# Kernel tuning notes

Hardware: AMD Instinct MI355X
Metric: run time of the kernel (lower is better)

## Reference

```python
import jax, jax.numpy as jnp
import numpy as np

N_NODES = 50000
N_EDGES = 500000
D_NODE = 128
D_EDGE = 64
D_HID = 256
D_OUT = 64


def setup_inputs() -> dict:
    key = jax.random.key(0)
    k1, k2, k3, k4, k5 = jax.random.split(key, 5)
    node_feats = jax.random.normal(k1, (N_NODES, D_NODE), dtype=jnp.float32)
    edge_index = jax.random.randint(k2, (2, N_EDGES), 0, N_NODES, dtype=jnp.int64)
    edge_attr = jax.random.normal(k3, (N_EDGES, D_EDGE), dtype=jnp.float32)
    d_in = 2 * D_NODE + D_EDGE  # 320
    W1 = jax.random.normal(k4, (d_in, D_HID), dtype=jnp.float32) * (1.0 / np.sqrt(d_in))
    b1 = jnp.zeros((D_HID,), dtype=jnp.float32)
    W2 = jax.random.normal(k5, (D_HID, D_OUT), dtype=jnp.float32) * (1.0 / np.sqrt(D_HID))
    b2 = jnp.zeros((D_OUT,), dtype=jnp.float32)
    return {"node_feats": node_feats, "edge_index": edge_index, "edge_attr": edge_attr,
            "W1": W1, "b1": b1, "W2": W2, "b2": b2}


def reference(node_feats, edge_index, edge_attr, W1, b1, W2, b2):
    row, col = edge_index[0], edge_index[1]
    # irregular gather of endpoint features, concat with edge attrs: [E, 2*d_node + d_edge]
    x = jnp.concatenate([node_feats[row], node_feats[col], edge_attr], axis=1)
    h = jax.nn.relu(x @ W1 + b1)  # [E, D_HID]
    return h @ W2 + b2            # [E, D_OUT]
```

## Files before the change

### kernel.cpp

```cpp
#include <hip/hip_runtime.h>
#include <hip/hip_bf16.h>
#include <stdint.h>

#define E_EDGES 500000
#define NNODES  50000
#define DN 128
#define DE 64
#define DH 256
#define DO 64
#define BE 32

typedef __attribute__((ext_vector_type(8))) short short8;
typedef __attribute__((ext_vector_type(4))) short short4v;
typedef __attribute__((ext_vector_type(4))) float f32x4;

__device__ __forceinline__ short f2bf(float f) {
    union { float f; uint32_t u; } v; v.f = f;
    uint32_t r = (v.u + 0x7FFFu + ((v.u >> 16) & 1u)) >> 16;
    return (short)(uint16_t)r;
}
__device__ __forceinline__ float bf2f(short s) {
    union { uint32_t u; float f; } v; v.u = ((uint32_t)(uint16_t)s) << 16;
    return v.f;
}

__global__ void convert_weights(const float* __restrict__ W1, const float* __restrict__ W2,
                                short* __restrict__ WcatT, short* __restrict__ W1cT,
                                short* __restrict__ W2T) {
    int idx = blockIdx.x * 256 + threadIdx.x;
    if (idx < 512 * 128) {
        int c = idx >> 7, k = idx & 127;
        WcatT[idx] = f2bf(W1[(c < 256 ? k : k + 128) * DH + (c & 255)]);
    } else if (idx < 512 * 128 + 256 * 64) {
        int i = idx - 512 * 128;
        int c = i >> 6, k = i & 63;
        W1cT[i] = f2bf(W1[(256 + k) * DH + c]);
    } else if (idx < 512 * 128 + 256 * 64 + 64 * 256) {
        int i = idx - 512 * 128 - 256 * 64;
        int n = i >> 8, k = i & 255;
        W2T[i] = f2bf(W2[k * DO + n]);
    }
}

__global__ __launch_bounds__(256, 4) void node_gemm(
    const float* __restrict__ nf, const short* __restrict__ WcatT, short* __restrict__ PQ)
{
    __shared__ __align__(16) short xt[64 * 128];
    const int tid = threadIdx.x, lane = tid & 63, wv = tid >> 6;
    const int lr = lane & 15, lk = lane >> 4;
    const int r0 = blockIdx.x * 64;
    const int cb = blockIdx.y * 256;
    char* xb = (char*)xt;

    {
        int r = tid >> 2, q = tid & 3;
        int gr = r0 + r; if (gr > NNODES - 1) gr = NNODES - 1;
        const float4* src = (const float4*)(nf + (long)gr * DN) + q * 8;
        #pragma unroll
        for (int i = 0; i < 4; ++i) {
            float4 a = src[2 * i], b = src[2 * i + 1];
            short8 s = { f2bf(a.x), f2bf(a.y), f2bf(a.z), f2bf(a.w),
                         f2bf(b.x), f2bf(b.y), f2bf(b.z), f2bf(b.w) };
            *(short8*)(xb + ((r * 256 + q * 64 + i * 16) ^ ((r & 7) << 4))) = s;
        }
    }
    __syncthreads();

    f32x4 acc[4][4];
    #pragma unroll
    for (int m = 0; m < 4; ++m)
        #pragma unroll
        for (int n = 0; n < 4; ++n)
            acc[m][n] = (f32x4){0.f, 0.f, 0.f, 0.f};

    #pragma unroll
    for (int kt = 0; kt < 4; ++kt) {
        short8 a[4], w[4];
        #pragma unroll
        for (int m = 0; m < 4; ++m) {
            int row = 16 * m + lr;
            a[m] = *(const short8*)(xb + ((row * 256 + kt * 64 + lk * 16) ^ ((row & 7) << 4)));
        }
        #pragma unroll
        for (int n = 0; n < 4; ++n)
            w[n] = *(const short8*)(WcatT + (long)(cb + wv * 64 + n * 16 + lr) * 128 + kt * 32 + lk * 8);
        #pragma unroll
        for (int m = 0; m < 4; ++m)
            #pragma unroll
            for (int n = 0; n < 4; ++n)
                acc[m][n] = __builtin_amdgcn_mfma_f32_16x16x32_bf16(w[n], a[m], acc[m][n], 0, 0, 0);
    }

    #pragma unroll
    for (int m = 0; m < 4; ++m) {
        int row = r0 + 16 * m + lr;
        if (row < NNODES) {
            #pragma unroll
            for (int n = 0; n < 4; ++n) {
                short4v s = { f2bf(acc[m][n][0]), f2bf(acc[m][n][1]),
                              f2bf(acc[m][n][2]), f2bf(acc[m][n][3]) };
                *(short4v*)(PQ + (long)row * 512 + cb + wv * 64 + n * 16 + lk * 4) = s;
            }
        }
    }
}

__global__ __launch_bounds__(256, 6) void edge_mlp(
    const int* __restrict__ eidx, const float* __restrict__ ea,
    const short* __restrict__ PQ, const short* __restrict__ W1cT,
    const float* __restrict__ b1, const short* __restrict__ W2T,
    const float* __restrict__ b2, float* __restrict__ out)
{
    __shared__ __align__(16) short st[BE * 256];
    const int tid = threadIdx.x, lane = tid & 63, wv = tid >> 6;
    const int lr = lane & 15, lk = lane >> 4;
    const long e0 = (long)blockIdx.x * BE;
    char* sb = (char*)st;

    {
        int e = tid >> 3, r = tid & 7;
        long ge = e0 + e;
        int ri = eidx[ge];
        int ci = eidx[E_EDGES + ge];
        const short8* ps = (const short8*)(PQ + (long)ri * 512) + r * 4;
        const short8* qs = (const short8*)(PQ + (long)ci * 512 + 256) + r * 4;
        #pragma unroll
        for (int i = 0; i < 4; ++i) {
            short8 p = ps[i], q = qs[i];
            short8 s;
            #pragma unroll
            for (int j = 0; j < 8; ++j)
                s[j] = f2bf(bf2f(p[j]) + bf2f(q[j]));
            *(short8*)(sb + ((e * 512 + r * 64 + i * 16) ^ ((e & 7) << 4))) = s;
        }
    }
    __syncthreads();

    f32x4 acc[2][4];
    #pragma unroll
    for (int m = 0; m < 2; ++m)
        #pragma unroll
        for (int n = 0; n < 4; ++n)
            acc[m][n] = (f32x4){0.f, 0.f, 0.f, 0.f};

    #pragma unroll
    for (int kt = 0; kt < 2; ++kt) {
        short8 w[4], eb[2];
        #pragma unroll
        for (int n = 0; n < 4; ++n)
            w[n] = *(const short8*)(W1cT + (wv * 64 + n * 16 + lr) * 64 + kt * 32 + lk * 8);
        #pragma unroll
        for (int m = 0; m < 2; ++m) {
            const float4* s = (const float4*)(ea + (e0 + 16 * m + lr) * DE + kt * 32 + lk * 8);
            float4 x = s[0], y = s[1];
            eb[m] = (short8){ f2bf(x.x), f2bf(x.y), f2bf(x.z), f2bf(x.w),
                              f2bf(y.x), f2bf(y.y), f2bf(y.z), f2bf(y.w) };
        }
        #pragma unroll
        for (int m = 0; m < 2; ++m)
            #pragma unroll
            for (int n = 0; n < 4; ++n)
                acc[m][n] = __builtin_amdgcn_mfma_f32_16x16x32_bf16(w[n], eb[m], acc[m][n], 0, 0, 0);
    }

    #pragma unroll
    for (int n = 0; n < 4; ++n) {
        float4 bb = *(const float4*)(b1 + wv * 64 + n * 16 + lk * 4);
        #pragma unroll
        for (int m = 0; m < 2; ++m) {
            int e = 16 * m + lr;
            int hc = wv * 64 + n * 16 + lk * 4;
            char* addr = sb + ((e * 512 + hc * 2) ^ ((e & 7) << 4));
            short4v s = *(short4v*)addr;
            short4v hb;
            hb.x = f2bf(fmaxf(acc[m][n][0] + bb.x + bf2f(s.x), 0.f));
            hb.y = f2bf(fmaxf(acc[m][n][1] + bb.y + bf2f(s.y), 0.f));
            hb.z = f2bf(fmaxf(acc[m][n][2] + bb.z + bf2f(s.z), 0.f));
            hb.w = f2bf(fmaxf(acc[m][n][3] + bb.w + bf2f(s.w), 0.f));
            *(short4v*)addr = hb;
        }
    }
    __syncthreads();

    f32x4 acc2[2];
    acc2[0] = (f32x4){0.f, 0.f, 0.f, 0.f};
    acc2[1] = (f32x4){0.f, 0.f, 0.f, 0.f};

    #pragma unroll
    for (int kt = 0; kt < 8; ++kt) {
        short8 w2 = *(const short8*)(W2T + (wv * 16 + lr) * 256 + kt * 32 + lk * 8);
        #pragma unroll
        for (int m = 0; m < 2; ++m) {
            int e = 16 * m + lr;
            short8 hb = *(const short8*)(sb + ((e * 512 + kt * 64 + lk * 16) ^ ((e & 7) << 4)));
            acc2[m] = __builtin_amdgcn_mfma_f32_16x16x32_bf16(w2, hb, acc2[m], 0, 0, 0);
        }
    }

    #pragma unroll
    for (int m = 0; m < 2; ++m) {
        float4 bb = *(const float4*)(b2 + wv * 16 + lk * 4);
        long ge = e0 + 16 * m + lr;
        float4 o;
        o.x = acc2[m][0] + bb.x;
        o.y = acc2[m][1] + bb.y;
        o.z = acc2[m][2] + bb.z;
        o.w = acc2[m][3] + bb.w;
        *(float4*)(out + ge * DO + wv * 16 + lk * 4) = o;
    }
}

extern "C" void kernel_launch(void* const* d_in, const int* in_sizes, int n_in,
                              void* d_out, int out_size, void* d_ws, size_t ws_size,
                              hipStream_t stream) {
    const float* node_feats = (const float*)d_in[0];
    const int*   eidx       = (const int*)d_in[1];
    const float* edge_attr  = (const float*)d_in[2];
    const float* W1         = (const float*)d_in[3];
    const float* b1         = (const float*)d_in[4];
    const float* W2         = (const float*)d_in[5];
    const float* b2         = (const float*)d_in[6];
    float* out = (float*)d_out;

    short* WcatT = (short*)d_ws;
    short* W1cT  = WcatT + 512 * 128;
    short* W2T   = W1cT + 256 * 64;
    short* PQ    = W2T + 64 * 256;

    convert_weights<<<384, 256, 0, stream>>>(W1, W2, WcatT, W1cT, W2T);
    node_gemm<<<dim3(782, 2), 256, 0, stream>>>(node_feats, WcatT, PQ);
    edge_mlp<<<E_EDGES / BE, 256, 0, stream>>>(eidx, edge_attr, PQ, W1cT, b1, W2T, b2, out);
}
```

Baseline: 267.6 us.

## Gather node projections straight into MFMA accumulators and fold b1 into node GEMM

The edge kernel now loads the gathered P and Q projection slices directly into the per-lane accumulator layout, summing them in fp32 to initialise the first-layer MFMA accumulators. This removes the shared-memory staging pass, one barrier, and an extra bf16 round-trip. Bias b1 is added once per node in the node GEMM, not once per edge, and the hidden activations go into a padded, non-swizzled shared layout matched to the second GEMM's reads. The trade is narrower (8-byte) scattered global loads per lane in place of 16-byte row loads.

```diff
diff --git a/kernel.cpp b/kernel.cpp
--- a/kernel.cpp
+++ b/kernel.cpp
@@ -9,19 +9,16 @@
 #define DH 256
 #define DO 64
 #define BE 32
+#define TS 528
 
 typedef __attribute__((ext_vector_type(8))) short short8;
 typedef __attribute__((ext_vector_type(4))) short short4v;
 typedef __attribute__((ext_vector_type(4))) float f32x4;
 
 __device__ __forceinline__ short f2bf(float f) {
-    union { float f; uint32_t u; } v; v.f = f;
-    uint32_t r = (v.u + 0x7FFFu + ((v.u >> 16) & 1u)) >> 16;
-    return (short)(uint16_t)r;
-}
-__device__ __forceinline__ float bf2f(short s) {
-    union { uint32_t u; float f; } v; v.u = ((uint32_t)(uint16_t)s) << 16;
-    return v.f;
+    union { __hip_bfloat16 h; short s; } u;
+    u.h = __float2bfloat16(f);
+    return u.s;
 }
 
 __global__ void convert_weights(const float* __restrict__ W1, const float* __restrict__ W2,
@@ -43,7 +40,8 @@
 }
 
 __global__ __launch_bounds__(256, 4) void node_gemm(
-    const float* __restrict__ nf, const short* __restrict__ WcatT, short* __restrict__ PQ)
+    const float* __restrict__ nf, const short* __restrict__ WcatT,
+    const float* __restrict__ b1, short* __restrict__ PQ)
 {
     __shared__ __align__(16) short xt[64 * 128];
     const int tid = threadIdx.x, lane = tid & 63, wv = tid >> 6;
@@ -97,51 +95,52 @@
         if (row < NNODES) {
             #pragma unroll
             for (int n = 0; n < 4; ++n) {
-                short4v s = { f2bf(acc[m][n][0]), f2bf(acc[m][n][1]),
-                              f2bf(acc[m][n][2]), f2bf(acc[m][n][3]) };
+                float4 bv = make_float4(0.f, 0.f, 0.f, 0.f);
+                if (cb == 0) bv = *(const float4*)(b1 + wv * 64 + n * 16 + lk * 4);
+                short4v s = { f2bf(acc[m][n][0] + bv.x), f2bf(acc[m][n][1] + bv.y),
+                              f2bf(acc[m][n][2] + bv.z), f2bf(acc[m][n][3] + bv.w) };
                 *(short4v*)(PQ + (long)row * 512 + cb + wv * 64 + n * 16 + lk * 4) = s;
             }
         }
     }
+}
+
+__device__ __forceinline__ f32x4 pq_add(uint2 p, uint2 q) {
+    union { uint32_t u; float f; } a, b;
+    f32x4 r;
+    a.u = p.x << 16;          b.u = q.x << 16;          r[0] = a.f + b.f;
+    a.u = p.x & 0xffff0000u;  b.u = q.x & 0xffff0000u;  r[1] = a.f + b.f;
+    a.u = p.y << 16;          b.u = q.y << 16;          r[2] = a.f + b.f;
+    a.u = p.y & 0xffff0000u;  b.u = q.y & 0xffff0000u;  r[3] = a.f + b.f;
+    return r;
 }
 
 __global__ __launch_bounds__(256, 6) void edge_mlp(
     const int* __restrict__ eidx, const float* __restrict__ ea,
     const short* __restrict__ PQ, const short* __restrict__ W1cT,
-    const float* __restrict__ b1, const short* __restrict__ W2T,
-    const float* __restrict__ b2, float* __restrict__ out)
+    const short* __restrict__ W2T, const float* __restrict__ b2,
+    float* __restrict__ out)
 {
-    __shared__ __align__(16) short st[BE * 256];
+    __shared__ __align__(16) char hbuf[32 * TS];
+
     const int tid = threadIdx.x, lane = tid & 63, wv = tid >> 6;
     const int lr = lane & 15, lk = lane >> 4;
     const long e0 = (long)blockIdx.x * BE;
-    char* sb = (char*)st;
-
-    {
-        int e = tid >> 3, r = tid & 7;
-        long ge = e0 + e;
-        int ri = eidx[ge];
-        int ci = eidx[E_EDGES + ge];
-        const short8* ps = (const short8*)(PQ + (long)ri * 512) + r * 4;
-        const short8* qs = (const short8*)(PQ + (long)ci * 512 + 256) + r * 4;
-        #pragma unroll
-        for (int i = 0; i < 4; ++i) {
-            short8 p = ps[i], q = qs[i];
-            short8 s;
-            #pragma unroll
-            for (int j = 0; j < 8; ++j)
-                s[j] = f2bf(bf2f(p[j]) + bf2f(q[j]));
-            *(short8*)(sb + ((e * 512 + r * 64 + i * 16) ^ ((e & 7) << 4))) = s;
-        }
-    }
-    __syncthreads();
+
+    const int ri0 = eidx[e0 + lr],      ci0 = eidx[E_EDGES + e0 + lr];
+    const int ri1 = eidx[e0 + 16 + lr], ci1 = eidx[E_EDGES + e0 + 16 + lr];
 
     f32x4 acc[2][4];
-    #pragma unroll
-    for (int m = 0; m < 2; ++m)
-        #pragma unroll
-        for (int n = 0; n < 4; ++n)
-            acc[m][n] = (f32x4){0.f, 0.f, 0.f, 0.f};
+    const int hcb = wv * 64 + lk * 4;
+    #pragma unroll
+    for (int n = 0; n < 4; ++n) {
+        uint2 p0 = *(const uint2*)(PQ + (long)ri0 * 512 + hcb + n * 16);
+        uint2 q0 = *(const uint2*)(PQ + (long)ci0 * 512 + 256 + hcb + n * 16);
+        uint2 p1 = *(const uint2*)(PQ + (long)ri1 * 512 + hcb + n * 16);
+        uint2 q1 = *(const uint2*)(PQ + (long)ci1 * 512 + 256 + hcb + n * 16);
+        acc[0][n] = pq_add(p0, q0);
+        acc[1][n] = pq_add(p1, q1);
+    }
 
     #pragma unroll
     for (int kt = 0; kt < 2; ++kt) {
@@ -164,20 +163,16 @@
     }
 
     #pragma unroll
-    for (int n = 0; n < 4; ++n) {
-        float4 bb = *(const float4*)(b1 + wv * 64 + n * 16 + lk * 4);
-        #pragma unroll
-        for (int m = 0; m < 2; ++m) {
-            int e = 16 * m + lr;
-            int hc = wv * 64 + n * 16 + lk * 4;
-            char* addr = sb + ((e * 512 + hc * 2) ^ ((e & 7) << 4));
-            short4v s = *(short4v*)addr;
-            short4v hb;
-            hb.x = f2bf(fmaxf(acc[m][n][0] + bb.x + bf2f(s.x), 0.f));
-            hb.y = f2bf(fmaxf(acc[m][n][1] + bb.y + bf2f(s.y), 0.f));
-            hb.z = f2bf(fmaxf(acc[m][n][2] + bb.z + bf2f(s.z), 0.f));
-            hb.w = f2bf(fmaxf(acc[m][n][3] + bb.w + bf2f(s.w), 0.f));
-            *(short4v*)addr = hb;
+    for (int m = 0; m < 2; ++m) {
+        const int e = 16 * m + lr;
+        #pragma unroll
+        for (int n = 0; n < 4; ++n) {
+            const int o = 8 * wv + 2 * n + (lk >> 1);
+            short4v hs = { f2bf(fmaxf(acc[m][n][0], 0.f)),
+                           f2bf(fmaxf(acc[m][n][1], 0.f)),
+                           f2bf(fmaxf(acc[m][n][2], 0.f)),
+                           f2bf(fmaxf(acc[m][n][3], 0.f)) };
+            *(short4v*)(hbuf + o * TS + e * 16 + (lk & 1) * 8) = hs;
         }
     }
     __syncthreads();
@@ -191,15 +186,14 @@
         short8 w2 = *(const short8*)(W2T + (wv * 16 + lr) * 256 + kt * 32 + lk * 8);
         #pragma unroll
         for (int m = 0; m < 2; ++m) {
-            int e = 16 * m + lr;
-            short8 hb = *(const short8*)(sb + ((e * 512 + kt * 64 + lk * 16) ^ ((e & 7) << 4)));
+            short8 hb = *(const short8*)(hbuf + (4 * kt + lk) * TS + (16 * m + lr) * 16);
             acc2[m] = __builtin_amdgcn_mfma_f32_16x16x32_bf16(w2, hb, acc2[m], 0, 0, 0);
         }
     }
 
+    float4 bb = *(const float4*)(b2 + wv * 16 + lk * 4);
     #pragma unroll
     for (int m = 0; m < 2; ++m) {
-        float4 bb = *(const float4*)(b2 + wv * 16 + lk * 4);
         long ge = e0 + 16 * m + lr;
         float4 o;
         o.x = acc2[m][0] + bb.x;
@@ -228,6 +222,6 @@
     short* PQ    = W2T + 64 * 256;
 
     convert_weights<<<384, 256, 0, stream>>>(W1, W2, WcatT, W1cT, W2T);
-    node_gemm<<<dim3(782, 2), 256, 0, stream>>>(node_feats, WcatT, PQ);
-    edge_mlp<<<E_EDGES / BE, 256, 0, stream>>>(eidx, edge_attr, PQ, W1cT, b1, W2T, b2, out);
-}
+    node_gemm<<<dim3(782, 2), 256, 0, stream>>>(node_feats, WcatT, b1, PQ);
+    edge_mlp<<<E_EDGES / BE, 256, 0, stream>>>(eidx, edge_attr, PQ, W1cT, W2T, b2, out);
+}
```

New measurement: 335.2 us. 1.25x slower.
